# Kernel tuning notes

Hardware: AMD Instinct MI355X
Metric: run time of the kernel (lower is better)

Reference implementation:

```python
import jax, jax.numpy as jnp
import numpy as np

B, N, D, K = 128, 512, 512, 8

def setup_inputs() -> dict:
    key = jax.random.key(0)
    ks = jax.random.split(key, 6)
    coefficients = jax.random.normal(ks[0], (B, N, D), dtype=jnp.float32)
    H = D // 2
    s1 = 1.0 / np.sqrt(D)
    s2 = 1.0 / np.sqrt(H)
    W1 = jax.random.uniform(ks[1], (D, H), jnp.float32, -s1, s1)
    b1 = jax.random.uniform(ks[2], (H,), jnp.float32, -s1, s1)
    W2 = jax.random.uniform(ks[3], (H,), jnp.float32, -s2, s2)
    b2 = jax.random.uniform(ks[4], (), jnp.float32, -s2, s2)
    base_logits = jnp.zeros((N,), jnp.float32)  # nn.Parameter(torch.zeros(n_freqs))
    return {"coefficients": coefficients, "W1": W1, "b1": b1, "W2": W2, "b2": b2,
            "base_logits": base_logits}

def reference(coefficients, W1, b1, W2, b2, base_logits):
    # scorer: Linear(D, D//2) -> GELU(exact) -> Linear(D//2, 1), squeeze last dim
    h = jax.nn.gelu(jnp.einsum('bnd,dh->bnh', coefficients, W1) + b1, approximate=False)
    logits = jnp.einsum('bnh,h->bn', h, W2) + b2 + base_logits[None, :]  # (B, N)
    # inference path (self.training == False): plain softmax, no gumbel noise
    probs = jax.nn.softmax(logits, axis=-1)
    _, indices = jax.lax.top_k(probs, K)                      # (B, K) int32
    mask = jnp.zeros_like(probs).at[jnp.arange(B)[:, None], indices].set(1.0)
    selected = jnp.take_along_axis(coefficients, indices[:, :, None], axis=1)  # (B, K, D)
    importance = probs  # softmax(logits) again in torch; identical in eval mode
    return selected, mask, importance, indices
```

## Files before the change

### kernel.cpp

```cpp
#include <hip/hip_runtime.h>
#include <math.h>

#define B_DIM 128
#define N_DIM 512
#define D_DIM 512
#define H_DIM 256
#define K_SEL 8

typedef _Float16 half8 __attribute__((ext_vector_type(8)));
typedef float    f32x4 __attribute__((ext_vector_type(4)));

__global__ __launch_bounds__(512) void prep_w1_kernel(
    const float* __restrict__ W1,
    _Float16* __restrict__ w1frag_h,
    _Float16* __restrict__ w1frag_l)
{
    const int b    = blockIdx.x;
    const int c4   = b >> 4;
    const int ks   = b & 15;
    const int lane = threadIdx.x >> 3;
    const int j    = threadIdx.x & 7;
    const int col  = c4 * 16 + (lane & 15);
    const int k    = ks * 32 + (lane >> 4) * 8 + j;
    float x = W1[(size_t)k * H_DIM + col];
    _Float16 h = (_Float16)x;
    float r = x - (float)h;
    size_t o = (size_t)b * 512 + lane * 8 + j;
    w1frag_h[o] = h;
    w1frag_l[o] = (_Float16)(r * 2048.0f);
}

__global__ __launch_bounds__(512, 2) void fused_scorer_mfma(
    const float* __restrict__ X,
    const _Float16* __restrict__ w1frag_h,
    const _Float16* __restrict__ w1frag_l,
    const float* __restrict__ b1,
    const float* __restrict__ W2,
    float* __restrict__ lp)
{
    __shared__ half8 Ah[2][1024], Al[2][1024];

    const int tid  = threadIdx.x;
    const int lane = tid & 63;
    const int wave = tid >> 6;
    const int wm   = (wave >> 1) << 6;
    const int wnx  = wave & 1;
    const int l15  = lane & 15;
    const int lg   = lane >> 4;
    const int rowtile = blockIdx.x & 255;
    const int colhalf = blockIdx.x >> 8;
    const int row0 = rowtile * 256;
    const int c4base = colhalf * 8 + wnx * 4;

    const int rc  = tid & 255;
    const int kc1 = tid >> 8;
    const float* xp = X + (size_t)(row0 + rc) * D_DIM + kc1 * 8;

    const _Float16* fbh_base = w1frag_h + (size_t)lane * 8;
    const _Float16* fbl_base = w1frag_l + (size_t)lane * 8;

    f32x4 acc[4][4];
    #pragma unroll
    for (int mi = 0; mi < 4; ++mi)
        #pragma unroll
        for (int nj = 0; nj < 4; ++nj)
            acc[mi][nj] = (f32x4){0.f, 0.f, 0.f, 0.f};

    float4 xv[4];
    auto load_a = [&](int k0) {
        xv[0] = *reinterpret_cast<const float4*>(xp + k0);
        xv[1] = *reinterpret_cast<const float4*>(xp + k0 + 4);
        xv[2] = *reinterpret_cast<const float4*>(xp + k0 + 16);
        xv[3] = *reinterpret_cast<const float4*>(xp + k0 + 20);
    };
    auto split_write = [&](int buf) {
        #pragma unroll
        for (int q = 0; q < 2; ++q) {
            float e[8] = {xv[2*q].x, xv[2*q].y, xv[2*q].z, xv[2*q].w,
                          xv[2*q+1].x, xv[2*q+1].y, xv[2*q+1].z, xv[2*q+1].w};
            half8 hh, ll;
            #pragma unroll
            for (int j = 0; j < 8; ++j) {
                _Float16 h = (_Float16)e[j];
                float r = e[j] - (float)h;
                hh[j] = h;
                ll[j] = (_Float16)(r * 2048.0f);
            }
            Ah[buf][tid + q * 512] = hh;
            Al[buf][tid + q * 512] = ll;
        }
    };

    load_a(0);
    split_write(0);
    load_a(32);
    __syncthreads();

    for (int ks = 0; ks < 16; ++ks) {
        const int buf = ks & 1, nbuf = buf ^ 1;
        if (ks < 15) {
            split_write(nbuf);
            if (ks < 14) load_a((ks + 2) * 32);
        }
        #pragma unroll
        for (int p = 0; p < 2; ++p) {
            half8 fah[2], fal[2];
            #pragma unroll
            for (int m = 0; m < 2; ++m) {
                int ca = lg * 256 + wm + (p * 2 + m) * 16 + l15;
                fah[m] = Ah[buf][ca];
                fal[m] = Al[buf][ca];
            }
            #pragma unroll
            for (int nj = 0; nj < 4; ++nj) {
                size_t fo = (size_t)(((c4base + nj) * 16 + ks)) << 9;
                half8 fbh = *reinterpret_cast<const half8*>(fbh_base + fo);
                half8 fbl = *reinterpret_cast<const half8*>(fbl_base + fo);
                #pragma unroll
                for (int m = 0; m < 2; ++m) {
                    int mi = p * 2 + m;
                    acc[mi][nj] = __builtin_amdgcn_mfma_f32_16x16x32_f16(fah[m], fbh, acc[mi][nj], 0, 0, 0);
                    f32x4 t = __builtin_amdgcn_mfma_f32_16x16x32_f16(fah[m], fbl, (f32x4){0.f,0.f,0.f,0.f}, 0, 0, 0);
                    t = __builtin_amdgcn_mfma_f32_16x16x32_f16(fal[m], fbh, t, 0, 0, 0);
                    acc[mi][nj] += t * (1.0f / 2048.0f);
                }
            }
        }
        __syncthreads();
    }

    float b1v[4], w2v[4];
    #pragma unroll
    for (int nj = 0; nj < 4; ++nj) {
        int col = colhalf * 128 + wnx * 64 + nj * 16 + l15;
        b1v[nj] = b1[col];
        w2v[nj] = W2[col];
    }
    float part[4][4];
    #pragma unroll
    for (int mi = 0; mi < 4; ++mi)
        #pragma unroll
        for (int r = 0; r < 4; ++r)
            part[mi][r] = 0.f;
    #pragma unroll
    for (int mi = 0; mi < 4; ++mi)
        #pragma unroll
        for (int nj = 0; nj < 4; ++nj)
            #pragma unroll
            for (int r = 0; r < 4; ++r) {
                float z = acc[mi][nj][r] + b1v[nj];
                float g = 0.5f * z * (1.0f + erff(z * 0.70710678118654752440f));
                part[mi][r] = fmaf(g, w2v[nj], part[mi][r]);
            }
    float* red = reinterpret_cast<float*>(&Ah[0][0]);
    #pragma unroll
    for (int mi = 0; mi < 4; ++mi)
        #pragma unroll
        for (int r = 0; r < 4; ++r) {
            float v = part[mi][r];
            v += __shfl_xor(v, 1, 16);
            v += __shfl_xor(v, 2, 16);
            v += __shfl_xor(v, 4, 16);
            v += __shfl_xor(v, 8, 16);
            if (l15 == 0)
                red[wnx * 256 + wm + mi * 16 + lg * 4 + r] = v;
        }
    __syncthreads();
    if (tid < 256)
        lp[(size_t)colhalf * 65536 + row0 + tid] = red[tid] + red[256 + tid];
}

__global__ __launch_bounds__(256) void softmax_topk_kernel(
    const float* __restrict__ lp,
    const float* __restrict__ b2p,
    const float* __restrict__ base_logits,
    float* __restrict__ out_mask,
    float* __restrict__ out_importance,
    float* __restrict__ out_indices)
{
    const int b = blockIdx.x;
    const int tid = threadIdx.x;
    __shared__ float probs[N_DIM];
    __shared__ float redf[4];
    __shared__ int   redi[4];
    __shared__ int   sel_idx[K_SEL];

    const float b2v = b2p[0];
    int i0g = b * N_DIM + tid;
    int i1g = i0g + 256;
    float l0 = lp[i0g] + lp[65536 + i0g] + b2v + base_logits[tid];
    float l1 = lp[i1g] + lp[65536 + i1g] + b2v + base_logits[tid + 256];

    float m = fmaxf(l0, l1);
    #pragma unroll
    for (int s = 32; s >= 1; s >>= 1) m = fmaxf(m, __shfl_xor(m, s, 64));
    if ((tid & 63) == 0) redf[tid >> 6] = m;
    __syncthreads();
    float gm = fmaxf(fmaxf(redf[0], redf[1]), fmaxf(redf[2], redf[3]));
    __syncthreads();

    float e0 = expf(l0 - gm), e1 = expf(l1 - gm);
    float ssum = e0 + e1;
    #pragma unroll
    for (int s = 32; s >= 1; s >>= 1) ssum += __shfl_xor(ssum, s, 64);
    if ((tid & 63) == 0) redf[tid >> 6] = ssum;
    __syncthreads();
    float denom = redf[0] + redf[1] + redf[2] + redf[3];
    float p0 = e0 / denom, p1 = e1 / denom;
    probs[tid] = p0;
    probs[tid + 256] = p1;
    out_importance[b * N_DIM + tid] = p0;
    out_importance[b * N_DIM + tid + 256] = p1;
    __syncthreads();

    for (int it = 0; it < K_SEL; ++it) {
        float v0 = probs[tid]; int i0 = tid;
        float v1 = probs[tid + 256];
        if (v1 > v0) { v0 = v1; i0 = tid + 256; }
        #pragma unroll
        for (int s = 32; s >= 1; s >>= 1) {
            float ov = __shfl_xor(v0, s, 64);
            int   oi = __shfl_xor(i0, s, 64);
            if (ov > v0 || (ov == v0 && oi < i0)) { v0 = ov; i0 = oi; }
        }
        if ((tid & 63) == 0) { redf[tid >> 6] = v0; redi[tid >> 6] = i0; }
        __syncthreads();
        if (tid == 0) {
            float bv = redf[0]; int bi = redi[0];
            for (int w = 1; w < 4; ++w)
                if (redf[w] > bv || (redf[w] == bv && redi[w] < bi)) { bv = redf[w]; bi = redi[w]; }
            sel_idx[it] = bi;
            probs[bi] = -1.0f;
        }
        __syncthreads();
    }

    float mk0 = 0.f, mk1 = 0.f;
    #pragma unroll
    for (int i = 0; i < K_SEL; ++i) {
        if (sel_idx[i] == tid)       mk0 = 1.f;
        if (sel_idx[i] == tid + 256) mk1 = 1.f;
    }
    out_mask[b * N_DIM + tid] = mk0;
    out_mask[b * N_DIM + tid + 256] = mk1;

    if (tid < K_SEL) out_indices[b * K_SEL + tid] = (float)sel_idx[tid];
}

__global__ __launch_bounds__(256) void gather_kernel(
    const float* __restrict__ X,
    const float* __restrict__ out_indices,
    float* __restrict__ out_selected)
{
    const int b = blockIdx.x;
    const int tid = threadIdx.x;
    __shared__ int sel[K_SEL];
    if (tid < K_SEL) sel[tid] = (int)out_indices[b * K_SEL + tid];
    __syncthreads();
    #pragma unroll
    for (int i = 0; i < 4; ++i) {
        int f = tid + 256 * i;
        int ki = f >> 7;
        int c4 = f & 127;
        float4 v = reinterpret_cast<const float4*>(
            X + ((size_t)b * N_DIM + sel[ki]) * D_DIM)[c4];
        reinterpret_cast<float4*>(
            out_selected + ((size_t)b * K_SEL + ki) * D_DIM)[c4] = v;
    }
}

extern "C" void kernel_launch(void* const* d_in, const int* in_sizes, int n_in,
                              void* d_out, int out_size, void* d_ws, size_t ws_size,
                              hipStream_t stream) {
    const float* X           = (const float*)d_in[0];
    const float* W1          = (const float*)d_in[1];
    const float* b1          = (const float*)d_in[2];
    const float* W2          = (const float*)d_in[3];
    const float* b2          = (const float*)d_in[4];
    const float* base_logits = (const float*)d_in[5];

    float* out            = (float*)d_out;
    float* out_selected   = out;
    float* out_mask       = out_selected + B_DIM * K_SEL * D_DIM;
    float* out_importance = out_mask + B_DIM * N_DIM;
    float* out_indices    = out_importance + B_DIM * N_DIM;

    float*    lp       = out_selected;
    _Float16* w1frag_h = (_Float16*)(out_selected + 131072);
    _Float16* w1frag_l = (_Float16*)(out_selected + 196608);

    hipLaunchKernelGGL(prep_w1_kernel, dim3(256), dim3(512), 0, stream,
                       W1, w1frag_h, w1frag_l);
    hipLaunchKernelGGL(fused_scorer_mfma, dim3(512), dim3(512), 0, stream,
                       X, w1frag_h, w1frag_l, b1, W2, lp);
    hipLaunchKernelGGL(softmax_topk_kernel, dim3(B_DIM), dim3(256), 0, stream,
                       lp, b2, base_logits, out_mask, out_importance, out_indices);
    hipLaunchKernelGGL(gather_kernel, dim3(B_DIM), dim3(256), 0, stream,
                       X, out_indices, out_selected);
}
```

Measured before the change: 110.0 us.

## Stage W1 fragments into LDS via direct global-to-LDS loads, accumulate correction separately

W1 fragments are now loaded once per block with global_load_lds into double-buffered shared memory instead of each wave issuing its own global loads every k-step. The low-order correction products now go into a second accumulator that is scaled only once at the end, which removes the per-step scale-and-add and the zero-initialised temporary MFMA chain. The doubled accumulator register footprint forces the launch bound down to one block per CU, so fewer waves are left to hide latency.

```diff
diff --git a/kernel.cpp b/kernel.cpp
--- a/kernel.cpp
+++ b/kernel.cpp
@@ -9,6 +9,11 @@
 
 typedef _Float16 half8 __attribute__((ext_vector_type(8)));
 typedef float    f32x4 __attribute__((ext_vector_type(4)));
+
+__device__ __forceinline__ void gload_lds16(const void* g, void* l) {
+    __builtin_amdgcn_global_load_lds((const __attribute__((address_space(1))) void*)g,
+                                     (__attribute__((address_space(3))) void*)l, 16, 0, 0);
+}
 
 __global__ __launch_bounds__(512) void prep_w1_kernel(
     const float* __restrict__ W1,
@@ -30,7 +35,7 @@
     w1frag_l[o] = (_Float16)(r * 2048.0f);
 }
 
-__global__ __launch_bounds__(512, 2) void fused_scorer_mfma(
+__global__ __launch_bounds__(512, 1) void fused_scorer_mfma(
     const float* __restrict__ X,
     const _Float16* __restrict__ w1frag_h,
     const _Float16* __restrict__ w1frag_l,
@@ -39,6 +44,7 @@
     float* __restrict__ lp)
 {
     __shared__ half8 Ah[2][1024], Al[2][1024];
+    __shared__ half8 Bh[2][512],  Bl[2][512];
 
     const int tid  = threadIdx.x;
     const int lane = tid & 63;
@@ -50,21 +56,22 @@
     const int rowtile = blockIdx.x & 255;
     const int colhalf = blockIdx.x >> 8;
     const int row0 = rowtile * 256;
-    const int c4base = colhalf * 8 + wnx * 4;
 
     const int rc  = tid & 255;
     const int kc1 = tid >> 8;
     const float* xp = X + (size_t)(row0 + rc) * D_DIM + kc1 * 8;
 
-    const _Float16* fbh_base = w1frag_h + (size_t)lane * 8;
-    const _Float16* fbl_base = w1frag_l + (size_t)lane * 8;
-
-    f32x4 acc[4][4];
+    const _Float16* bsrc_h = w1frag_h + ((size_t)(colhalf * 8 + (tid >> 6)) * 16) * 512 + (tid & 63) * 8;
+    const _Float16* bsrc_l = w1frag_l + ((size_t)(colhalf * 8 + (tid >> 6)) * 16) * 512 + (tid & 63) * 8;
+
+    f32x4 acc[4][4], acc2[4][4];
     #pragma unroll
     for (int mi = 0; mi < 4; ++mi)
         #pragma unroll
-        for (int nj = 0; nj < 4; ++nj)
-            acc[mi][nj] = (f32x4){0.f, 0.f, 0.f, 0.f};
+        for (int nj = 0; nj < 4; ++nj) {
+            acc[mi][nj]  = (f32x4){0.f, 0.f, 0.f, 0.f};
+            acc2[mi][nj] = (f32x4){0.f, 0.f, 0.f, 0.f};
+        }
 
     float4 xv[4];
     auto load_a = [&](int k0) {
@@ -90,8 +97,13 @@
             Al[buf][tid + q * 512] = ll;
         }
     };
+    auto stage_b = [&](int buf, int ks) {
+        gload_lds16(bsrc_h + (size_t)ks * 512, &Bh[buf][tid]);
+        gload_lds16(bsrc_l + (size_t)ks * 512, &Bl[buf][tid]);
+    };
 
     load_a(0);
+    stage_b(0, 0);
     split_write(0);
     load_a(32);
     __syncthreads();
@@ -99,8 +111,16 @@
     for (int ks = 0; ks < 16; ++ks) {
         const int buf = ks & 1, nbuf = buf ^ 1;
         if (ks < 15) {
+            stage_b(nbuf, ks + 1);
             split_write(nbuf);
             if (ks < 14) load_a((ks + 2) * 32);
+        }
+        half8 fbh[4], fbl[4];
+        #pragma unroll
+        for (int nj = 0; nj < 4; ++nj) {
+            int cb = (wnx * 4 + nj) * 64 + lane;
+            fbh[nj] = Bh[buf][cb];
+            fbl[nj] = Bl[buf][cb];
         }
         #pragma unroll
         for (int p = 0; p < 2; ++p) {
@@ -112,19 +132,14 @@
                 fal[m] = Al[buf][ca];
             }
             #pragma unroll
-            for (int nj = 0; nj < 4; ++nj) {
-                size_t fo = (size_t)(((c4base + nj) * 16 + ks)) << 9;
-                half8 fbh = *reinterpret_cast<const half8*>(fbh_base + fo);
-                half8 fbl = *reinterpret_cast<const half8*>(fbl_base + fo);
+            for (int nj = 0; nj < 4; ++nj)
                 #pragma unroll
                 for (int m = 0; m < 2; ++m) {
                     int mi = p * 2 + m;
-                    acc[mi][nj] = __builtin_amdgcn_mfma_f32_16x16x32_f16(fah[m], fbh, acc[mi][nj], 0, 0, 0);
-                    f32x4 t = __builtin_amdgcn_mfma_f32_16x16x32_f16(fah[m], fbl, (f32x4){0.f,0.f,0.f,0.f}, 0, 0, 0);
-                    t = __builtin_amdgcn_mfma_f32_16x16x32_f16(fal[m], fbh, t, 0, 0, 0);
-                    acc[mi][nj] += t * (1.0f / 2048.0f);
+                    acc[mi][nj]  = __builtin_amdgcn_mfma_f32_16x16x32_f16(fah[m], fbh[nj], acc[mi][nj],  0, 0, 0);
+                    acc2[mi][nj] = __builtin_amdgcn_mfma_f32_16x16x32_f16(fah[m], fbl[nj], acc2[mi][nj], 0, 0, 0);
+                    acc2[mi][nj] = __builtin_amdgcn_mfma_f32_16x16x32_f16(fal[m], fbh[nj], acc2[mi][nj], 0, 0, 0);
                 }
-            }
         }
         __syncthreads();
     }
@@ -148,7 +163,7 @@
         for (int nj = 0; nj < 4; ++nj)
             #pragma unroll
             for (int r = 0; r < 4; ++r) {
-                float z = acc[mi][nj][r] + b1v[nj];
+                float z = acc[mi][nj][r] + acc2[mi][nj][r] * (1.0f / 2048.0f) + b1v[nj];
                 float g = 0.5f * z * (1.0f + erff(z * 0.70710678118654752440f));
                 part[mi][r] = fmaf(g, w2v[nj], part[mi][r]);
             }
```

Result: no change. 110.9 us (+0.8%).

## Stage W1 quarter slices in LDS and stream X fragments straight into registers

Applied to the files above, without the earlier changes.

The scorer kernel now splits the hidden dimension into four quarters per block and loads the whole W1 fragment slice for that quarter into LDS once with global_load_lds. Each wave streams its own 32 tokens of X directly from global memory into registers and splits them to fp16 hi/lo without a shared-memory staging pass. This removes the per-k-step barriers and the repeated global W1 fragment loads. The correction-term MFMAs now accumulate into a separate accumulator that is rescaled only once at the end. The trade-off is that X is read four times, once per quarter instead of twice, there are four partial-logit planes to sum in the softmax kernel, and the 128KB LDS footprint forces one block per CU.

```diff
diff --git a/kernel.cpp b/kernel.cpp
--- a/kernel.cpp
+++ b/kernel.cpp
@@ -9,6 +9,11 @@
 
 typedef _Float16 half8 __attribute__((ext_vector_type(8)));
 typedef float    f32x4 __attribute__((ext_vector_type(4)));
+
+__device__ __forceinline__ void gload_lds16(const void* g, void* l) {
+    __builtin_amdgcn_global_load_lds((const __attribute__((address_space(1))) void*)g,
+                                     (__attribute__((address_space(3))) void*)l, 16, 0, 0);
+}
 
 __global__ __launch_bounds__(512) void prep_w1_kernel(
     const float* __restrict__ W1,
@@ -30,7 +35,7 @@
     w1frag_l[o] = (_Float16)(r * 2048.0f);
 }
 
-__global__ __launch_bounds__(512, 2) void fused_scorer_mfma(
+__global__ __launch_bounds__(512, 1) void fused_scorer_wlds(
     const float* __restrict__ X,
     const _Float16* __restrict__ w1frag_h,
     const _Float16* __restrict__ w1frag_l,
@@ -38,136 +43,110 @@
     const float* __restrict__ W2,
     float* __restrict__ lp)
 {
-    __shared__ half8 Ah[2][1024], Al[2][1024];
+    __shared__ half8 Wh[4096], Wl[4096];
 
     const int tid  = threadIdx.x;
     const int lane = tid & 63;
     const int wave = tid >> 6;
-    const int wm   = (wave >> 1) << 6;
-    const int wnx  = wave & 1;
     const int l15  = lane & 15;
     const int lg   = lane >> 4;
-    const int rowtile = blockIdx.x & 255;
-    const int colhalf = blockIdx.x >> 8;
-    const int row0 = rowtile * 256;
-    const int c4base = colhalf * 8 + wnx * 4;
-
-    const int rc  = tid & 255;
-    const int kc1 = tid >> 8;
-    const float* xp = X + (size_t)(row0 + rc) * D_DIM + kc1 * 8;
-
-    const _Float16* fbh_base = w1frag_h + (size_t)lane * 8;
-    const _Float16* fbl_base = w1frag_l + (size_t)lane * 8;
-
-    f32x4 acc[4][4];
-    #pragma unroll
-    for (int mi = 0; mi < 4; ++mi)
-        #pragma unroll
-        for (int nj = 0; nj < 4; ++nj)
-            acc[mi][nj] = (f32x4){0.f, 0.f, 0.f, 0.f};
-
-    float4 xv[4];
-    auto load_a = [&](int k0) {
-        xv[0] = *reinterpret_cast<const float4*>(xp + k0);
-        xv[1] = *reinterpret_cast<const float4*>(xp + k0 + 4);
-        xv[2] = *reinterpret_cast<const float4*>(xp + k0 + 16);
-        xv[3] = *reinterpret_cast<const float4*>(xp + k0 + 20);
+    const int quarter = blockIdx.x >> 8;
+    const int wgq     = blockIdx.x & 255;
+    const int tok0 = (wgq * 8 + wave) * 32;
+
+    #pragma unroll
+    for (int c = wave; c < 64; c += 8) {
+        size_t so = ((size_t)(quarter * 64 + c)) * 512 + lane * 8;
+        gload_lds16(w1frag_h + so, &Wh[c * 64 + lane]);
+        gload_lds16(w1frag_l + so, &Wl[c * 64 + lane]);
+    }
+
+    f32x4 acc[4][2], acc2[4][2];
+    #pragma unroll
+    for (int m = 0; m < 4; ++m)
+        #pragma unroll
+        for (int tg = 0; tg < 2; ++tg) {
+            acc[m][tg]  = (f32x4){0.f, 0.f, 0.f, 0.f};
+            acc2[m][tg] = (f32x4){0.f, 0.f, 0.f, 0.f};
+        }
+
+    const float* xp0 = X + (size_t)(tok0 + l15) * D_DIM + lg * 8;
+    const float* xp1 = xp0 + (size_t)16 * D_DIM;
+
+    auto split8 = [&](float4 a, float4 b, half8& hh, half8& ll) {
+        float e[8] = {a.x, a.y, a.z, a.w, b.x, b.y, b.z, b.w};
+        #pragma unroll
+        for (int j = 0; j < 8; ++j) {
+            _Float16 h = (_Float16)e[j];
+            float r = e[j] - (float)h;
+            hh[j] = h;
+            ll[j] = (_Float16)(r * 2048.0f);
+        }
     };
-    auto split_write = [&](int buf) {
-        #pragma unroll
-        for (int q = 0; q < 2; ++q) {
-            float e[8] = {xv[2*q].x, xv[2*q].y, xv[2*q].z, xv[2*q].w,
-                          xv[2*q+1].x, xv[2*q+1].y, xv[2*q+1].z, xv[2*q+1].w};
-            half8 hh, ll;
+
+    float4 xv[2][2][2];
+    xv[0][0][0] = *reinterpret_cast<const float4*>(xp0);
+    xv[0][0][1] = *reinterpret_cast<const float4*>(xp0 + 4);
+    xv[0][1][0] = *reinterpret_cast<const float4*>(xp1);
+    xv[0][1][1] = *reinterpret_cast<const float4*>(xp1 + 4);
+    xv[1][0][0] = *reinterpret_cast<const float4*>(xp0 + 32);
+    xv[1][0][1] = *reinterpret_cast<const float4*>(xp0 + 36);
+    xv[1][1][0] = *reinterpret_cast<const float4*>(xp1 + 32);
+    xv[1][1][1] = *reinterpret_cast<const float4*>(xp1 + 36);
+
+    __syncthreads();
+
+    for (int ks = 0; ks < 16; ++ks) {
+        const int buf = ks & 1;
+        half8 bxh[2], bxl[2];
+        split8(xv[buf][0][0], xv[buf][0][1], bxh[0], bxl[0]);
+        split8(xv[buf][1][0], xv[buf][1][1], bxh[1], bxl[1]);
+        if (ks < 14) {
+            const int ko = (ks + 2) * 32;
+            xv[buf][0][0] = *reinterpret_cast<const float4*>(xp0 + ko);
+            xv[buf][0][1] = *reinterpret_cast<const float4*>(xp0 + ko + 4);
+            xv[buf][1][0] = *reinterpret_cast<const float4*>(xp1 + ko);
+            xv[buf][1][1] = *reinterpret_cast<const float4*>(xp1 + ko + 4);
+        }
+        #pragma unroll
+        for (int m = 0; m < 4; ++m) {
+            const int c = (m * 16 + ks) * 64 + lane;
+            half8 wh = Wh[c];
+            half8 wl = Wl[c];
             #pragma unroll
-            for (int j = 0; j < 8; ++j) {
-                _Float16 h = (_Float16)e[j];
-                float r = e[j] - (float)h;
-                hh[j] = h;
-                ll[j] = (_Float16)(r * 2048.0f);
+            for (int tg = 0; tg < 2; ++tg) {
+                acc[m][tg]  = __builtin_amdgcn_mfma_f32_16x16x32_f16(wh, bxh[tg], acc[m][tg],  0, 0, 0);
+                acc2[m][tg] = __builtin_amdgcn_mfma_f32_16x16x32_f16(wh, bxl[tg], acc2[m][tg], 0, 0, 0);
+                acc2[m][tg] = __builtin_amdgcn_mfma_f32_16x16x32_f16(wl, bxh[tg], acc2[m][tg], 0, 0, 0);
             }
-            Ah[buf][tid + q * 512] = hh;
-            Al[buf][tid + q * 512] = ll;
-        }
-    };
-
-    load_a(0);
-    split_write(0);
-    load_a(32);
-    __syncthreads();
-
-    for (int ks = 0; ks < 16; ++ks) {
-        const int buf = ks & 1, nbuf = buf ^ 1;
-        if (ks < 15) {
-            split_write(nbuf);
-            if (ks < 14) load_a((ks + 2) * 32);
-        }
-        #pragma unroll
-        for (int p = 0; p < 2; ++p) {
-            half8 fah[2], fal[2];
-            #pragma unroll
-            for (int m = 0; m < 2; ++m) {
-                int ca = lg * 256 + wm + (p * 2 + m) * 16 + l15;
-                fah[m] = Ah[buf][ca];
-                fal[m] = Al[buf][ca];
-            }
-            #pragma unroll
-            for (int nj = 0; nj < 4; ++nj) {
-                size_t fo = (size_t)(((c4base + nj) * 16 + ks)) << 9;
-                half8 fbh = *reinterpret_cast<const half8*>(fbh_base + fo);
-                half8 fbl = *reinterpret_cast<const half8*>(fbl_base + fo);
-                #pragma unroll
-                for (int m = 0; m < 2; ++m) {
-                    int mi = p * 2 + m;
-                    acc[mi][nj] = __builtin_amdgcn_mfma_f32_16x16x32_f16(fah[m], fbh, acc[mi][nj], 0, 0, 0);
-                    f32x4 t = __builtin_amdgcn_mfma_f32_16x16x32_f16(fah[m], fbl, (f32x4){0.f,0.f,0.f,0.f}, 0, 0, 0);
-                    t = __builtin_amdgcn_mfma_f32_16x16x32_f16(fal[m], fbh, t, 0, 0, 0);
-                    acc[mi][nj] += t * (1.0f / 2048.0f);
-                }
-            }
-        }
-        __syncthreads();
-    }
-
-    float b1v[4], w2v[4];
-    #pragma unroll
-    for (int nj = 0; nj < 4; ++nj) {
-        int col = colhalf * 128 + wnx * 64 + nj * 16 + l15;
-        b1v[nj] = b1[col];
-        w2v[nj] = W2[col];
-    }
-    float part[4][4];
-    #pragma unroll
-    for (int mi = 0; mi < 4; ++mi)
-        #pragma unroll
-        for (int r = 0; r < 4; ++r)
-            part[mi][r] = 0.f;
-    #pragma unroll
-    for (int mi = 0; mi < 4; ++mi)
-        #pragma unroll
-        for (int nj = 0; nj < 4; ++nj)
+        }
+    }
+
+    float part[2] = {0.f, 0.f};
+    #pragma unroll
+    for (int m = 0; m < 4; ++m) {
+        const int col4 = quarter * 64 + m * 16 + lg * 4;
+        float4 b1v = *reinterpret_cast<const float4*>(b1 + col4);
+        float4 w2v = *reinterpret_cast<const float4*>(W2 + col4);
+        float bb[4] = {b1v.x, b1v.y, b1v.z, b1v.w};
+        float ww[4] = {w2v.x, w2v.y, w2v.z, w2v.w};
+        #pragma unroll
+        for (int tg = 0; tg < 2; ++tg)
             #pragma unroll
             for (int r = 0; r < 4; ++r) {
-                float z = acc[mi][nj][r] + b1v[nj];
+                float z = acc[m][tg][r] + acc2[m][tg][r] * (1.0f / 2048.0f) + bb[r];
                 float g = 0.5f * z * (1.0f + erff(z * 0.70710678118654752440f));
-                part[mi][r] = fmaf(g, w2v[nj], part[mi][r]);
+                part[tg] = fmaf(g, ww[r], part[tg]);
             }
-    float* red = reinterpret_cast<float*>(&Ah[0][0]);
-    #pragma unroll
-    for (int mi = 0; mi < 4; ++mi)
-        #pragma unroll
-        for (int r = 0; r < 4; ++r) {
-            float v = part[mi][r];
-            v += __shfl_xor(v, 1, 16);
-            v += __shfl_xor(v, 2, 16);
-            v += __shfl_xor(v, 4, 16);
-            v += __shfl_xor(v, 8, 16);
-            if (l15 == 0)
-                red[wnx * 256 + wm + mi * 16 + lg * 4 + r] = v;
-        }
-    __syncthreads();
-    if (tid < 256)
-        lp[(size_t)colhalf * 65536 + row0 + tid] = red[tid] + red[256 + tid];
+    }
+    #pragma unroll
+    for (int tg = 0; tg < 2; ++tg) {
+        float v = part[tg];
+        v += __shfl_xor(v, 16, 64);
+        v += __shfl_xor(v, 32, 64);
+        if (lane < 16)
+            lp[(size_t)quarter * 65536 + tok0 + tg * 16 + lane] = v;
+    }
 }
 
 __global__ __launch_bounds__(256) void softmax_topk_kernel(
@@ -188,8 +167,10 @@
     const float b2v = b2p[0];
     int i0g = b * N_DIM + tid;
     int i1g = i0g + 256;
-    float l0 = lp[i0g] + lp[65536 + i0g] + b2v + base_logits[tid];
-    float l1 = lp[i1g] + lp[65536 + i1g] + b2v + base_logits[tid + 256];
+    float l0 = (lp[i0g] + lp[65536 + i0g]) + (lp[131072 + i0g] + lp[196608 + i0g]);
+    float l1 = (lp[i1g] + lp[65536 + i1g]) + (lp[131072 + i1g] + lp[196608 + i1g]);
+    l0 += b2v + base_logits[tid];
+    l1 += b2v + base_logits[tid + 256];
 
     float m = fmaxf(l0, l1);
     #pragma unroll
@@ -286,12 +267,12 @@
     float* out_indices    = out_importance + B_DIM * N_DIM;
 
     float*    lp       = out_selected;
-    _Float16* w1frag_h = (_Float16*)(out_selected + 131072);
-    _Float16* w1frag_l = (_Float16*)(out_selected + 196608);
+    _Float16* w1frag_h = (_Float16*)(out_selected + 262144);
+    _Float16* w1frag_l = (_Float16*)(out_selected + 327680);
 
     hipLaunchKernelGGL(prep_w1_kernel, dim3(256), dim3(512), 0, stream,
                        W1, w1frag_h, w1frag_l);
-    hipLaunchKernelGGL(fused_scorer_mfma, dim3(512), dim3(512), 0, stream,
+    hipLaunchKernelGGL(fused_scorer_wlds, dim3(1024), dim3(512), 0, stream,
                        X, w1frag_h, w1frag_l, b1, W2, lp);
     hipLaunchKernelGGL(softmax_topk_kernel, dim3(B_DIM), dim3(256), 0, stream,
                        lp, b2, base_logits, out_mask, out_importance, out_indices);
```

After: 211.2 us. +91.9%, slower.
